# Kernel tuning notes

Hardware: AMD Instinct MI355X
Metric: run time of the kernel (lower is better)

Reference implementation:

```python
import jax, jax.numpy as jnp
import numpy as np

B, N, D = 4096, 64, 256  # batch, n_nodes, d_input


def setup_inputs() -> dict:
    key = jax.random.key(0)
    k = jax.random.split(key, 6)
    return {
        "x": jax.random.normal(k[0], (B, N, D), dtype=jnp.float32),
        "W1": jax.random.normal(k[1], (1,), dtype=jnp.float32),
        "W2": jax.random.normal(k[2], (D, 1), dtype=jnp.float32),
        "W3": jax.random.normal(k[3], (D,), dtype=jnp.float32),
        "bs": jax.random.normal(k[4], (1, N, N), dtype=jnp.float32),
        "Vs": jax.random.normal(k[5], (N, N), dtype=jnp.float32),
    }


def reference(x, W1, W2, W3, bs, Vs):
    # x: (B, N, D). Dropout is identity (inference / p=0).
    # LHS = (x * W1) @ W2  -> (B, N, 1); collapse to (B, N)
    lhs = jnp.einsum("bnd,d->bn", x, W2[:, 0]) * W1[0]
    # RHS = W3 @ x (over feature dim) -> (B, N); used as (B, 1, N)
    rhs = jnp.einsum("bnd,d->bn", x, W3)
    # scores: Vs @ tanh(outer(lhs, rhs) + bs)  -> (B, N, N)
    t = jnp.tanh(lhs[:, :, None] * rhs[:, None, :] + bs)  # (B, N, N)
    s = jnp.einsum("ij,bjk->bik", Vs, t)  # (B, N, N)
    # softmax over the flattened N*N scores per batch element
    a = jax.nn.softmax(s.reshape(x.shape[0], -1), axis=-1)
    return a.reshape(-1, N, N)
```

## Files before the change

kernel.cpp:

```cpp
#include <hip/hip_runtime.h>


typedef float f32x4 __attribute__((ext_vector_type(4)));
typedef float f32x2 __attribute__((ext_vector_type(2)));
typedef __bf16 bf16x8 __attribute__((ext_vector_type(8)));

__global__ __launch_bounds__(256, 4) void adjatt_kernel(
    const float* __restrict__ x,
    const float* __restrict__ W1,
    const float* __restrict__ W2,
    const float* __restrict__ W3,
    const float* __restrict__ bs,
    const float* __restrict__ Vs,
    float* __restrict__ out)
{
    __shared__ __align__(16) unsigned char tT[16384];
    __shared__ __align__(16) float lhs[64];
    __shared__ __align__(16) float rhs[64];
    __shared__ f32x2 red[4];

    const int tid  = threadIdx.x;
    const int b    = blockIdx.x;
    const int lane = tid & 63;
    const int w    = tid >> 6;
    const int l15  = lane & 15;
    const int g    = lane >> 4;

    const float W1v = W1[0];

    float bsv[16];
    {
        const int j0 = 16 * w;
        #pragma unroll
        for (int jj = 0; jj < 16; ++jj) bsv[jj] = bs[(j0 + jj) * 64 + lane];
    }

    bf16x8 Vh[2], Vl[2];
    {
        const int row = 16 * w + l15;
        #pragma unroll
        for (int sk = 0; sk < 2; ++sk) {
            const float* vp = Vs + row * 64 + 32 * sk + 8 * g;
            f32x4 f0 = *(const f32x4*)vp;
            f32x4 f1 = *(const f32x4*)(vp + 4);
            #pragma unroll
            for (int e = 0; e < 4; ++e) {
                __bf16 h0 = (__bf16)f0[e];
                Vh[sk][e] = h0;
                Vl[sk][e] = (__bf16)(f0[e] - (float)h0);
                __bf16 h1 = (__bf16)f1[e];
                Vh[sk][e + 4] = h1;
                Vl[sk][e + 4] = (__bf16)(f1[e] - (float)h1);
            }
        }
    }

    {
        const int co = tid & 15;
        const int r0 = tid >> 4;
        f32x4 w2v[4], w3v[4];
        #pragma unroll
        for (int kk = 0; kk < 4; ++kk) {
            w2v[kk] = *(const f32x4*)(W2 + 4 * (co + 16 * kk));
            w3v[kk] = *(const f32x4*)(W3 + 4 * (co + 16 * kk));
        }
        const float* xb = x + (size_t)b * 16384;
        #pragma unroll
        for (int it = 0; it < 4; ++it) {
            const int r = r0 + 16 * it;
            const float* xr = xb + r * 256;
            float d2 = 0.f, d3 = 0.f;
            #pragma unroll
            for (int kk = 0; kk < 4; ++kk) {
                f32x4 xv = *(const f32x4*)(xr + 4 * (co + 16 * kk));
                d2 = fmaf(xv[0], w2v[kk][0], d2); d2 = fmaf(xv[1], w2v[kk][1], d2);
                d2 = fmaf(xv[2], w2v[kk][2], d2); d2 = fmaf(xv[3], w2v[kk][3], d2);
                d3 = fmaf(xv[0], w3v[kk][0], d3); d3 = fmaf(xv[1], w3v[kk][1], d3);
                d3 = fmaf(xv[2], w3v[kk][2], d3); d3 = fmaf(xv[3], w3v[kk][3], d3);
            }
            d2 += __shfl_xor(d2, 1); d2 += __shfl_xor(d2, 2);
            d2 += __shfl_xor(d2, 4); d2 += __shfl_xor(d2, 8);
            d3 += __shfl_xor(d3, 1); d3 += __shfl_xor(d3, 2);
            d3 += __shfl_xor(d3, 4); d3 += __shfl_xor(d3, 8);
            if (co == 0) { lhs[r] = d2 * W1v; rhs[r] = d3; }
        }
    }
    __syncthreads();

    {
        const int n  = lane;
        const int j0 = 16 * w;
        const float rv = rhs[n];
        f32x4 lh[4];
        #pragma unroll
        for (int c = 0; c < 4; ++c) lh[c] = *(const f32x4*)&lhs[j0 + 4 * c];
        bf16x8 hi[2], lo[2];
        #pragma unroll
        for (int jj = 0; jj < 16; ++jj) {
            float z  = fmaf(lh[jj >> 2][jj & 3], rv, bsv[jj]);
            float e2 = __expf(2.f * z);
            float th = 1.f - __fdividef(2.f, e2 + 1.f);
            __bf16 h = (__bf16)th;
            hi[jj >> 3][jj & 7] = h;
            lo[jj >> 3][jj & 7] = (__bf16)(th - (float)h);
        }
        #pragma unroll
        for (int c = 0; c < 2; ++c) {
            const int off = (n * 128 + (j0 + 8 * c) * 2) ^ ((n & 7) << 4);
            *(bf16x8*)(tT + off)        = hi[c];
            *(bf16x8*)(tT + 8192 + off) = lo[c];
        }
    }
    __syncthreads();

    f32x4 acc[4];
    #pragma unroll
    for (int ct = 0; ct < 4; ++ct) acc[ct] = (f32x4){0.f, 0.f, 0.f, 0.f};
    #pragma unroll
    for (int ct = 0; ct < 4; ++ct) {
        const int n = 16 * ct + l15;
        #pragma unroll
        for (int sk = 0; sk < 2; ++sk) {
            const int off = (n * 128 + 64 * sk + 16 * g) ^ ((n & 7) << 4);
            bf16x8 Th = *(const bf16x8*)(tT + off);
            bf16x8 Tl = *(const bf16x8*)(tT + 8192 + off);
            acc[ct] = __builtin_amdgcn_mfma_f32_16x16x32_bf16(Th, Vh[sk], acc[ct], 0, 0, 0);
            acc[ct] = __builtin_amdgcn_mfma_f32_16x16x32_bf16(Tl, Vh[sk], acc[ct], 0, 0, 0);
            acc[ct] = __builtin_amdgcn_mfma_f32_16x16x32_bf16(Th, Vl[sk], acc[ct], 0, 0, 0);
        }
    }

    float m = acc[0][0];
    #pragma unroll
    for (int ct = 0; ct < 4; ++ct)
        #pragma unroll
        for (int e = 0; e < 4; ++e) m = fmaxf(m, acc[ct][e]);
    #pragma unroll
    for (int off = 1; off < 64; off <<= 1) m = fmaxf(m, __shfl_xor(m, off));
    float ssum = 0.f;
    #pragma unroll
    for (int ct = 0; ct < 4; ++ct)
        #pragma unroll
        for (int e = 0; e < 4; ++e) {
            acc[ct][e] = __expf(acc[ct][e] - m);
            ssum += acc[ct][e];
        }
    #pragma unroll
    for (int off = 1; off < 64; off <<= 1) ssum += __shfl_xor(ssum, off);
    if (lane == 0) red[w] = (f32x2){m, ssum};
    __syncthreads();
    const f32x2 r0v = red[0], r1v = red[1], r2v = red[2], r3v = red[3];
    const float M = fmaxf(fmaxf(r0v[0], r1v[0]), fmaxf(r2v[0], r3v[0]));
    const float S = r0v[1] * __expf(r0v[0] - M) + r1v[1] * __expf(r1v[0] - M) +
                    r2v[1] * __expf(r2v[0] - M) + r3v[1] * __expf(r3v[0] - M);
    const float f = __expf(m - M) * __fdividef(1.f, S);

    float* ob = out + (size_t)b * 4096 + (16 * w + l15) * 64 + 4 * g;
    #pragma unroll
    for (int ct = 0; ct < 4; ++ct) {
        f32x4 v = {acc[ct][0] * f, acc[ct][1] * f, acc[ct][2] * f, acc[ct][3] * f};
        *(f32x4*)(ob + 16 * ct) = v;
    }
}

extern "C" void kernel_launch(void* const* d_in, const int* in_sizes, int n_in,
                              void* d_out, int out_size, void* d_ws, size_t ws_size,
                              hipStream_t stream) {
    const float* x  = (const float*)d_in[0];
    const float* W1 = (const float*)d_in[1];
    const float* W2 = (const float*)d_in[2];
    const float* W3 = (const float*)d_in[3];
    const float* bs = (const float*)d_in[4];
    const float* Vs = (const float*)d_in[5];
    float* out = (float*)d_out;

    const int B = in_sizes[0] / (64 * 256);
    adjatt_kernel<<<dim3(B), dim3(256), 0, stream>>>(x, W1, W2, W3, bs, Vs, out);
}
```

Before: 68.92 us.

## Cut register pressure via LDS-staged weights and lazy bias loads, nontemporal stores

Stages W2/W3 in shared memory instead of holding 32 floats per thread in registers. Loads the bias values inside the tanh loop rather than prefetching 16 registers. Raises the launch-bounds occupancy hint from 4 to 6 blocks. Output is written with nontemporal stores to avoid polluting the cache. The aim is higher occupancy to hide memory latency on this bandwidth-bound kernel. The cost is an extra barrier, extra LDS reads, and bias loads now sitting on the critical path of the tanh loop.

```diff
diff --git a/kernel.cpp b/kernel.cpp
--- a/kernel.cpp
+++ b/kernel.cpp
@@ -5,7 +5,7 @@
 typedef float f32x2 __attribute__((ext_vector_type(2)));
 typedef __bf16 bf16x8 __attribute__((ext_vector_type(8)));
 
-__global__ __launch_bounds__(256, 4) void adjatt_kernel(
+__global__ __launch_bounds__(256, 6) void adjatt_kernel(
     const float* __restrict__ x,
     const float* __restrict__ W1,
     const float* __restrict__ W2,
@@ -15,6 +15,8 @@
     float* __restrict__ out)
 {
     __shared__ __align__(16) unsigned char tT[16384];
+    __shared__ __align__(16) float w2l[256];
+    __shared__ __align__(16) float w3l[256];
     __shared__ __align__(16) float lhs[64];
     __shared__ __align__(16) float rhs[64];
     __shared__ f32x2 red[4];
@@ -25,15 +27,13 @@
     const int w    = tid >> 6;
     const int l15  = lane & 15;
     const int g    = lane >> 4;
+    const int co   = tid & 15;
+    const int r0   = tid >> 4;
 
     const float W1v = W1[0];
 
-    float bsv[16];
-    {
-        const int j0 = 16 * w;
-        #pragma unroll
-        for (int jj = 0; jj < 16; ++jj) bsv[jj] = bs[(j0 + jj) * 64 + lane];
-    }
+    w2l[tid] = W2[tid];
+    w3l[tid] = W3[tid];
 
     bf16x8 Vh[2], Vl[2];
     {
@@ -54,16 +54,9 @@
             }
         }
     }
+    __syncthreads();
 
     {
-        const int co = tid & 15;
-        const int r0 = tid >> 4;
-        f32x4 w2v[4], w3v[4];
-        #pragma unroll
-        for (int kk = 0; kk < 4; ++kk) {
-            w2v[kk] = *(const f32x4*)(W2 + 4 * (co + 16 * kk));
-            w3v[kk] = *(const f32x4*)(W3 + 4 * (co + 16 * kk));
-        }
         const float* xb = x + (size_t)b * 16384;
         #pragma unroll
         for (int it = 0; it < 4; ++it) {
@@ -73,10 +66,12 @@
             #pragma unroll
             for (int kk = 0; kk < 4; ++kk) {
                 f32x4 xv = *(const f32x4*)(xr + 4 * (co + 16 * kk));
-                d2 = fmaf(xv[0], w2v[kk][0], d2); d2 = fmaf(xv[1], w2v[kk][1], d2);
-                d2 = fmaf(xv[2], w2v[kk][2], d2); d2 = fmaf(xv[3], w2v[kk][3], d2);
-                d3 = fmaf(xv[0], w3v[kk][0], d3); d3 = fmaf(xv[1], w3v[kk][1], d3);
-                d3 = fmaf(xv[2], w3v[kk][2], d3); d3 = fmaf(xv[3], w3v[kk][3], d3);
+                f32x4 w2 = *(const f32x4*)&w2l[4 * (co + 16 * kk)];
+                f32x4 w3 = *(const f32x4*)&w3l[4 * (co + 16 * kk)];
+                d2 = fmaf(xv[0], w2[0], d2); d2 = fmaf(xv[1], w2[1], d2);
+                d2 = fmaf(xv[2], w2[2], d2); d2 = fmaf(xv[3], w2[3], d2);
+                d3 = fmaf(xv[0], w3[0], d3); d3 = fmaf(xv[1], w3[1], d3);
+                d3 = fmaf(xv[2], w3[2], d3); d3 = fmaf(xv[3], w3[3], d3);
             }
             d2 += __shfl_xor(d2, 1); d2 += __shfl_xor(d2, 2);
             d2 += __shfl_xor(d2, 4); d2 += __shfl_xor(d2, 8);
@@ -97,7 +92,7 @@
         bf16x8 hi[2], lo[2];
         #pragma unroll
         for (int jj = 0; jj < 16; ++jj) {
-            float z  = fmaf(lh[jj >> 2][jj & 3], rv, bsv[jj]);
+            float z  = fmaf(lh[jj >> 2][jj & 3], rv, bs[(j0 + jj) * 64 + n]);
             float e2 = __expf(2.f * z);
             float th = 1.f - __fdividef(2.f, e2 + 1.f);
             __bf16 h = (__bf16)th;
@@ -106,7 +101,7 @@
         }
         #pragma unroll
         for (int c = 0; c < 2; ++c) {
-            const int off = (n * 128 + (j0 + 8 * c) * 2) ^ ((n & 7) << 4);
+            const int off = (lane * 128 + (j0 + 8 * c) * 2) ^ ((lane & 7) << 4);
             *(bf16x8*)(tT + off)        = hi[c];
             *(bf16x8*)(tT + 8192 + off) = lo[c];
         }
@@ -149,17 +144,17 @@
     for (int off = 1; off < 64; off <<= 1) ssum += __shfl_xor(ssum, off);
     if (lane == 0) red[w] = (f32x2){m, ssum};
     __syncthreads();
-    const f32x2 r0v = red[0], r1v = red[1], r2v = red[2], r3v = red[3];
-    const float M = fmaxf(fmaxf(r0v[0], r1v[0]), fmaxf(r2v[0], r3v[0]));
-    const float S = r0v[1] * __expf(r0v[0] - M) + r1v[1] * __expf(r1v[0] - M) +
-                    r2v[1] * __expf(r2v[0] - M) + r3v[1] * __expf(r3v[0] - M);
+    const f32x2 rv0 = red[0], rv1 = red[1], rv2 = red[2], rv3 = red[3];
+    const float M = fmaxf(fmaxf(rv0[0], rv1[0]), fmaxf(rv2[0], rv3[0]));
+    const float S = rv0[1] * __expf(rv0[0] - M) + rv1[1] * __expf(rv1[0] - M) +
+                    rv2[1] * __expf(rv2[0] - M) + rv3[1] * __expf(rv3[0] - M);
     const float f = __expf(m - M) * __fdividef(1.f, S);
 
     float* ob = out + (size_t)b * 4096 + (16 * w + l15) * 64 + 4 * g;
     #pragma unroll
     for (int ct = 0; ct < 4; ++ct) {
         f32x4 v = {acc[ct][0] * f, acc[ct][1] * f, acc[ct][2] * f, acc[ct][3] * f};
-        *(f32x4*)(ob + 16 * ct) = v;
+        __builtin_nontemporal_store(v, (f32x4*)(ob + 16 * ct));
     }
 }
 
```

Result: faster. 62.34 us (-9.5%).
